# Optimization experiments

Measured on AMD Instinct MI355X. Metric: run time of the kernel, lower is better.

Reference implementation:

```python
import jax, jax.numpy as jnp
import numpy as np

N_STEPS = 20  # ceil((t1-t0)/dt0) with dt0=0.05 on [0,1]


def setup_inputs() -> dict:
    key = jax.random.key(0)
    ks = jax.random.split(key, 12)
    B, D, H, VF, LS, LAB = 512, 5, 128, 256, 63, 10
    Lm1 = LS - 1  # 62, effective logsig dim after dropping channel 0
    ts = jnp.linspace(0.0, 1.0, 33, dtype=jnp.float32)
    intervals = jnp.linspace(0.0, 1.0, 33, dtype=jnp.float32)
    logsig = jax.random.normal(ks[0], (32, LS), dtype=jnp.float32)
    x0 = jax.random.normal(ks[1], (B, D), dtype=jnp.float32)
    def lin(k, fan_in, shape):
        return jax.random.uniform(k, shape, jnp.float32, -1.0, 1.0) / np.sqrt(fan_in)
    return {
        "ts": ts, "logsig": logsig, "x0": x0, "intervals": intervals,
        "W_vf1": lin(ks[2], H, (VF, H)),  "b_vf1": lin(ks[3], H, (VF,)),
        "W_vf2": lin(ks[4], VF, (VF, VF)), "b_vf2": lin(ks[5], VF, (VF,)),
        "W_m": lin(ks[6], VF, (H * Lm1, VF)), "b_m": lin(ks[7], VF, (H * Lm1,)),
        "W_in": lin(ks[8], D, (H, D)),   "b_in": lin(ks[9], D, (H,)),
        "W_out": lin(ks[10], H, (LAB, H)), "b_out": lin(ks[11], H, (LAB,)),
    }


def reference(ts, logsig, x0, intervals, W_vf1, b_vf1, W_vf2, b_vf2,
              W_m, b_m, W_in, b_in, W_out, b_out):
    B = x0.shape[0]
    H = W_in.shape[0]
    L = logsig.shape[1] - 1  # channel 0 dropped

    def vector_field(t, y):
        # locate interval containing t (torch.searchsorted default = left)
        idx = jnp.clip(jnp.searchsorted(intervals[1:], t) + 1, 1, intervals.shape[0] - 1)
        seg = logsig[idx - 1, 1:]                     # (L,)
        h = jax.nn.relu(y @ W_vf1.T + b_vf1)          # (B, VF)
        h = jnp.tanh(h @ W_vf2.T + b_vf2)             # (B, VF) final_activation=tanh
        m = (h @ W_m.T + b_m).reshape(B, H, L)        # (B, H, L)
        dydt = jnp.einsum('bhl,l->bh', m, seg)
        return dydt / (intervals[idx] - intervals[idx - 1])

    y0 = x0 @ W_in.T + b_in                           # linear1
    t0, t1 = ts[0], ts[-1]
    dt = (t1 - t0) / N_STEPS

    def heun_step(y, i):
        t = t0 + i * dt
        k1 = vector_field(t, y)
        k2 = vector_field(t + dt, y + dt * k1)
        return y + 0.5 * dt * (k1 + k2), None

    yT, _ = jax.lax.scan(heun_step, y0, jnp.arange(N_STEPS, dtype=jnp.float32))
    return jax.nn.softmax(yT @ W_out.T + b_out, axis=-1)
```

## Files before the change

### kernel.cpp

```cpp
#include <hip/hip_runtime.h>

#define YW 136

typedef _Float16 f16x8 __attribute__((ext_vector_type(8)));
typedef _Float16 f16x4 __attribute__((ext_vector_type(4)));
typedef __attribute__((ext_vector_type(4))) float f32x4;

__device__ __forceinline__ float fast_tanh(float x) {
    float e = __expf(2.0f * x);
    return 1.0f - 2.0f / (e + 1.0f);
}
__device__ __forceinline__ void bar_lds() {
    asm volatile("s_waitcnt lgkmcnt(0)\n\ts_barrier" ::: "memory");
}

__device__ __forceinline__ int fidx(int m, int c) {
    return ((c >> 5) << 9) | (((c >> 3) & 3) << 7) | (m << 3) | (c & 7);
}

__global__ __launch_bounds__(512) void pk_all(
    const float* __restrict__ Wvf1, const float* __restrict__ Wvf2,
    const float* __restrict__ Wm,   const float* __restrict__ bm,
    const float* __restrict__ logsig,
    _Float16* __restrict__ W1F, _Float16* __restrict__ W2F,
    _Float16* __restrict__ A3F, float* __restrict__ c_all)
{
    __shared__ float ls[8][62];
    const int b = blockIdx.x, t = threadIdx.x;
    if (b < 16) {
        int u0 = (b * 512 + t) * 4;
        int j0 = u0 & 7, l = (u0 >> 3) & 63;
        int kc = (u0 >> 9) & 3, nt = u0 >> 11;
        int n = nt * 16 + (l & 15), k0 = kc * 32 + (l >> 4) * 8 + j0;
        f32x4 w = *(const f32x4*)(Wvf1 + n * 128 + k0);
        f16x4 hv, lv;
#pragma unroll
        for (int c = 0; c < 4; c++) {
            _Float16 hi = (_Float16)w[c];
            hv[c] = hi;
            lv[c] = (_Float16)(w[c] - (float)hi);
        }
        *(f16x4*)(W1F + u0) = hv;
        *(f16x4*)(W1F + 32768 + u0) = lv;
    } else if (b < 48) {
        int u0 = ((b - 16) * 512 + t) * 4;
        int j0 = u0 & 7, l = (u0 >> 3) & 63;
        int kc = (u0 >> 9) & 7, nt = u0 >> 12;
        int n = nt * 16 + (l & 15), k0 = kc * 32 + (l >> 4) * 8 + j0;
        f32x4 w = *(const f32x4*)(Wvf2 + n * 256 + k0);
        f16x4 hv, lv;
#pragma unroll
        for (int c = 0; c < 4; c++) {
            _Float16 hi = (_Float16)w[c];
            hv[c] = hi;
            lv[c] = (_Float16)(w[c] - (float)hi);
        }
        *(f16x4*)(W2F + u0) = hv;
        *(f16x4*)(W2F + 65536 + u0) = lv;
    } else if (b < 112) {
        int tid = (b - 48) * 512 + t;
        int chunk = tid >> 13;
        int qi = tid & 8191;
        int u0 = qi * 4;
        int r0 = chunk * 8;
        for (int e2 = t; e2 < 8 * 62; e2 += 512)
            ls[e2 / 62][e2 % 62] = logsig[(r0 + e2 / 62) * 63 + 1 + (e2 % 62)];
        __syncthreads();
        int j0 = u0 & 7, l = (u0 >> 3) & 63, kc = (u0 >> 9) & 7, nt = (u0 >> 12) & 7;
        int h = nt * 16 + (l & 15);
        int v0 = kc * 32 + (l >> 4) * 8 + j0;
        f32x4 acc[8];
#pragma unroll
        for (int r = 0; r < 8; r++) acc[r] = (f32x4){0.f, 0.f, 0.f, 0.f};
        const float* wp = Wm + h * 62 * 256 + v0;
#pragma unroll 2
        for (int ll = 0; ll < 62; ll++) {
            f32x4 w4 = *(const f32x4*)(wp + ll * 256);
#pragma unroll
            for (int r = 0; r < 8; r++) {
                float lsv = ls[r][ll];
#pragma unroll
                for (int c = 0; c < 4; c++)
                    acc[r][c] += w4[c] * lsv;
            }
        }
#pragma unroll
        for (int r = 0; r < 8; r++) {
            f16x4 hv, lv;
#pragma unroll
            for (int c = 0; c < 4; c++) {
                _Float16 hi = (_Float16)acc[r][c];
                hv[c] = hi;
                lv[c] = (_Float16)(acc[r][c] - (float)hi);
            }
            *(f16x4*)(A3F + (r0 + r) * 65536 + u0) = hv;
            *(f16x4*)(A3F + (r0 + r) * 65536 + 32768 + u0) = lv;
        }
    } else {
        int u = (b - 112) * 512 + t;
        int r = u >> 7, h = u & 127;
        float acc = 0.f;
#pragma unroll
        for (int ll = 0; ll < 62; ll++) acc += bm[h * 62 + ll] * logsig[r * 63 + 1 + ll];
        c_all[u] = acc;
    }
}

__global__ __launch_bounds__(512, 2) void rde_main(
    const float* __restrict__ ts, const float* __restrict__ x0,
    const float* __restrict__ intervals,
    const float* __restrict__ b1g, const float* __restrict__ b2g,
    const float* __restrict__ Win, const float* __restrict__ bin,
    const float* __restrict__ Wout, const float* __restrict__ bout,
    const _Float16* __restrict__ W1F, const _Float16* __restrict__ W2F,
    const _Float16* __restrict__ A3F, const float* __restrict__ c_all,
    float* __restrict__ out)
{
    __shared__ __align__(16) _Float16 W1s[32768];
    __shared__ __align__(16) _Float16 H1h[4096];
    __shared__ __align__(16) _Float16 H2h[4096];
    __shared__ __align__(16) _Float16 Yh[2048];
    __shared__ __align__(16) _Float16 Yl[2048];
    __shared__ float ivl[33];
    __shared__ int   r_arr[40];
    __shared__ float s_arr[40];

    const int t    = threadIdx.x;
    const int lane = t & 63;
    const int wv   = t >> 6;
    const int m16  = lane & 15;
    const int q    = lane >> 4;
    const int row0 = blockIdx.x * 16;

    if (t < 33) ivl[t] = intervals[t];
    for (int e2 = t; e2 < 4096; e2 += 512)
        ((uint4*)W1s)[e2] = ((const uint4*)W1F)[e2];
    __syncthreads();

    const float ts0 = ts[0];
    const float dt  = __fdiv_rn(ts[32] - ts0, 20.0f);

    if (t < 40) {
        int i = t >> 1;
        float tv = ts0 + (float)i * dt;
        if (t & 1) tv += dt;
        int p = 0;
        for (int j2 = 0; j2 < 32; j2++) p += (ivl[1 + j2] < tv) ? 1 : 0;
        int idx = p + 1;
        idx = idx < 1 ? 1 : idx;
        idx = idx > 32 ? 32 : idx;
        r_arr[t] = idx - 1;
        s_arr[t] = __fdiv_rn(1.0f, ivl[idx] - ivl[idx - 1]);
    }

    f32x4 b1f[2], b2f[2];
#pragma unroll
    for (int tt = 0; tt < 2; tt++) {
        b1f[tt] = *(const f32x4*)(b1g + (wv * 2 + tt) * 16 + q * 4);
        b2f[tt] = *(const f32x4*)(b2g + (wv * 2 + tt) * 16 + q * 4);
    }

    float Y[4], K1[4];
    {
        const float* xr = x0 + (row0 + m16) * 5;
        float xv[5];
#pragma unroll
        for (int d = 0; d < 5; d++) xv[d] = xr[d];
        int c0 = wv * 16 + q * 4;
        f16x4 hv, lv;
#pragma unroll
        for (int r = 0; r < 4; r++) {
            float acc = bin[c0 + r];
#pragma unroll
            for (int d = 0; d < 5; d++) acc += xv[d] * Win[(c0 + r) * 5 + d];
            Y[r] = acc;
            K1[r] = 0.f;
            _Float16 hi = (_Float16)acc;
            hv[r] = hi;
            lv[r] = (_Float16)(acc - (float)hi);
        }
        *(f16x4*)(Yh + fidx(m16, c0)) = hv;
        *(f16x4*)(Yl + fidx(m16, c0)) = lv;
    }

    f16x8 w1lo[2][4];
#pragma unroll
    for (int tt = 0; tt < 2; tt++)
#pragma unroll
        for (int kc = 0; kc < 4; kc++)
            w1lo[tt][kc] = *(const f16x8*)(W1F + 32768 + ((wv * 8 + tt * 4 + kc) * 64 + lane) * 8);
    __syncthreads();

#pragma unroll 1
    for (int e = 0; e < 40; e++) {
        const int half = e & 1;
        const int ri   = r_arr[e];
        const float s  = s_arr[e];
        const _Float16* ABase = A3F + ri * 65536;

        f16x8 w2a[2][4][2];
#pragma unroll
        for (int tt = 0; tt < 2; tt++)
#pragma unroll
            for (int kc = 0; kc < 4; kc++) {
                const _Float16* bp = W2F + ((wv * 16 + tt * 8 + kc) * 64 + lane) * 8;
                w2a[tt][kc][0] = *(const f16x8*)bp;
                w2a[tt][kc][1] = *(const f16x8*)(bp + 65536);
            }
        f32x4 aA[2], aB[2], aC[2];
#pragma unroll
        for (int tt = 0; tt < 2; tt++) {
            aA[tt] = b1f[tt];
            aB[tt] = (f32x4){0.f, 0.f, 0.f, 0.f};
            aC[tt] = (f32x4){0.f, 0.f, 0.f, 0.f};
        }
#pragma unroll
        for (int kc = 0; kc < 4; kc++) {
            f16x8 ah = *(const f16x8*)(Yh + kc * 512 + lane * 8);
            f16x8 al = *(const f16x8*)(Yl + kc * 512 + lane * 8);
#pragma unroll
            for (int tt = 0; tt < 2; tt++) {
                f16x8 bh = *(const f16x8*)(W1s + ((wv * 8 + tt * 4 + kc) * 64 + lane) * 8);
                aA[tt] = __builtin_amdgcn_mfma_f32_16x16x32_f16(bh, ah, aA[tt], 0, 0, 0);
                aB[tt] = __builtin_amdgcn_mfma_f32_16x16x32_f16(w1lo[tt][kc], ah, aB[tt], 0, 0, 0);
                aC[tt] = __builtin_amdgcn_mfma_f32_16x16x32_f16(bh, al, aC[tt], 0, 0, 0);
            }
        }
#pragma unroll
        for (int tt = 0; tt < 2; tt++) {
            int n0 = (wv * 2 + tt) * 16 + q * 4;
            f16x4 hv;
#pragma unroll
            for (int r = 0; r < 4; r++)
                hv[r] = (_Float16)fmaxf(aA[tt][r] + aB[tt][r] + aC[tt][r], 0.f);
            *(f16x4*)(H1h + fidx(m16, n0)) = hv;
        }
        bar_lds();

        f16x8 w2b[2][4][2];
#pragma unroll
        for (int tt = 0; tt < 2; tt++)
#pragma unroll
            for (int kc = 0; kc < 4; kc++) {
                const _Float16* bp = W2F + ((wv * 16 + tt * 8 + 4 + kc) * 64 + lane) * 8;
                w2b[tt][kc][0] = *(const f16x8*)bp;
                w2b[tt][kc][1] = *(const f16x8*)(bp + 65536);
            }
#pragma unroll
        for (int tt = 0; tt < 2; tt++) {
            aA[tt] = b2f[tt];
            aB[tt] = (f32x4){0.f, 0.f, 0.f, 0.f};
        }
#pragma unroll
        for (int kc = 0; kc < 4; kc++) {
            f16x8 ah = *(const f16x8*)(H1h + kc * 512 + lane * 8);
#pragma unroll
            for (int tt = 0; tt < 2; tt++) {
                aA[tt] = __builtin_amdgcn_mfma_f32_16x16x32_f16(w2a[tt][kc][0], ah, aA[tt], 0, 0, 0);
                aB[tt] = __builtin_amdgcn_mfma_f32_16x16x32_f16(w2a[tt][kc][1], ah, aB[tt], 0, 0, 0);
            }
        }
        f16x8 a3a[4][2];
#pragma unroll
        for (int kc = 0; kc < 4; kc++) {
            const _Float16* bp = ABase + ((wv * 8 + kc) * 64 + lane) * 8;
            a3a[kc][0] = *(const f16x8*)bp;
            a3a[kc][1] = *(const f16x8*)(bp + 32768);
        }
        f32x4 cf = *(const f32x4*)(c_all + ri * 128 + wv * 16 + q * 4);
#pragma unroll
        for (int kc = 0; kc < 4; kc++) {
            f16x8 ah = *(const f16x8*)(H1h + (4 + kc) * 512 + lane * 8);
#pragma unroll
            for (int tt = 0; tt < 2; tt++) {
                aA[tt] = __builtin_amdgcn_mfma_f32_16x16x32_f16(w2b[tt][kc][0], ah, aA[tt], 0, 0, 0);
                aB[tt] = __builtin_amdgcn_mfma_f32_16x16x32_f16(w2b[tt][kc][1], ah, aB[tt], 0, 0, 0);
            }
        }
        f16x8 a3b[4][2];
#pragma unroll
        for (int kc = 0; kc < 4; kc++) {
            const _Float16* bp = ABase + ((wv * 8 + 4 + kc) * 64 + lane) * 8;
            a3b[kc][0] = *(const f16x8*)bp;
            a3b[kc][1] = *(const f16x8*)(bp + 32768);
        }
#pragma unroll
        for (int tt = 0; tt < 2; tt++) {
            int n0 = (wv * 2 + tt) * 16 + q * 4;
            f16x4 hv;
#pragma unroll
            for (int r = 0; r < 4; r++)
                hv[r] = (_Float16)fast_tanh(aA[tt][r] + aB[tt][r]);
            *(f16x4*)(H2h + fidx(m16, n0)) = hv;
        }
        bar_lds();

        f32x4 kA = cf;
        f32x4 kB = (f32x4){0.f, 0.f, 0.f, 0.f};
#pragma unroll
        for (int kc = 0; kc < 4; kc++) {
            f16x8 ah = *(const f16x8*)(H2h + kc * 512 + lane * 8);
            kA = __builtin_amdgcn_mfma_f32_16x16x32_f16(a3a[kc][0], ah, kA, 0, 0, 0);
            kB = __builtin_amdgcn_mfma_f32_16x16x32_f16(a3a[kc][1], ah, kB, 0, 0, 0);
        }
#pragma unroll
        for (int kc = 0; kc < 4; kc++) {
            f16x8 ah = *(const f16x8*)(H2h + (4 + kc) * 512 + lane * 8);
            kA = __builtin_amdgcn_mfma_f32_16x16x32_f16(a3b[kc][0], ah, kA, 0, 0, 0);
            kB = __builtin_amdgcn_mfma_f32_16x16x32_f16(a3b[kc][1], ah, kB, 0, 0, 0);
        }
#pragma unroll
        for (int tt = 0; tt < 2; tt++)
#pragma unroll
            for (int kc = 0; kc < 4; kc++)
                w1lo[tt][kc] = *(const f16x8*)(W1F + 32768 + ((wv * 8 + tt * 4 + kc) * 64 + lane) * 8);
        {
            int c0 = wv * 16 + q * 4;
            f16x4 hv, lv;
#pragma unroll
            for (int r = 0; r < 4; r++) {
                float kv = (kA[r] + kB[r]) * s;
                float yn;
                if (half == 0) {
                    K1[r] = kv;
                    yn = Y[r] + dt * kv;
                } else {
                    yn = Y[r] + 0.5f * dt * (K1[r] + kv);
                    Y[r] = yn;
                }
                _Float16 hi = (_Float16)yn;
                hv[r] = hi;
                lv[r] = (_Float16)(yn - (float)hi);
            }
            *(f16x4*)(Yh + fidx(m16, c0)) = hv;
            *(f16x4*)(Yl + fidx(m16, c0)) = lv;
        }
        bar_lds();
    }

    float* Ys  = (float*)&W1s[0];
    float* lgp = (float*)&W1s[0] + 16 * YW;
#pragma unroll
    for (int r = 0; r < 4; r++)
        Ys[m16 * YW + wv * 16 + q * 4 + r] = Y[r];
    __syncthreads();
    if (t < 160) {
        int m = t / 10, c = t % 10;
        float acc = bout[c];
        for (int k = 0; k < 128; k++) acc += Ys[m * YW + k] * Wout[c * 128 + k];
        lgp[m * 10 + c] = acc;
    }
    __syncthreads();
    if (t < 16) {
        float mx = -1e30f;
#pragma unroll
        for (int c = 0; c < 10; c++) mx = fmaxf(mx, lgp[t * 10 + c]);
        float ex[10], sum = 0.f;
#pragma unroll
        for (int c = 0; c < 10; c++) { ex[c] = expf(lgp[t * 10 + c] - mx); sum += ex[c]; }
        float inv = __fdiv_rn(1.0f, sum);
#pragma unroll
        for (int c = 0; c < 10; c++) out[(row0 + t) * 10 + c] = ex[c] * inv;
    }
}

extern "C" void kernel_launch(void* const* d_in, const int* in_sizes, int n_in,
                              void* d_out, int out_size, void* d_ws, size_t ws_size,
                              hipStream_t stream) {
    const float* ts     = (const float*)d_in[0];
    const float* logsig = (const float*)d_in[1];
    const float* x0     = (const float*)d_in[2];
    const float* ivls   = (const float*)d_in[3];
    const float* Wvf1   = (const float*)d_in[4];
    const float* bvf1   = (const float*)d_in[5];
    const float* Wvf2   = (const float*)d_in[6];
    const float* bvf2   = (const float*)d_in[7];
    const float* Wm     = (const float*)d_in[8];
    const float* bm     = (const float*)d_in[9];
    const float* Win    = (const float*)d_in[10];
    const float* bin    = (const float*)d_in[11];
    const float* Wout   = (const float*)d_in[12];
    const float* bout   = (const float*)d_in[13];

    _Float16* W1F = (_Float16*)d_ws;
    _Float16* W2F = W1F + 65536;
    _Float16* A3F = W2F + 131072;
    float* c_all = (float*)(A3F + 32 * 65536);
    float* out = (float*)d_out;

    pk_all<<<dim3(120), dim3(512), 0, stream>>>(Wvf1, Wvf2, Wm, bm, logsig,
                                                W1F, W2F, A3F, c_all);
    rde_main<<<dim3(32), dim3(512), 0, stream>>>(
        ts, x0, ivls, bvf1, bvf2, Win, bin, Wout, bout,
        W1F, W2F, A3F, c_all, out);
}
```

Measured before the change: 243.9 us.

## Fuse weight-packing prologue into main RDE kernel via cooperative grid sync

```diff
diff --git a/kernel.cpp b/kernel.cpp
--- a/kernel.cpp
+++ b/kernel.cpp
@@ -1,4 +1,7 @@
 #include <hip/hip_runtime.h>
+#include <hip/hip_cooperative_groups.h>
+
+namespace cg = cooperative_groups;
 
 #define YW 136
 
@@ -18,102 +21,17 @@
     return ((c >> 5) << 9) | (((c >> 3) & 3) << 7) | (m << 3) | (c & 7);
 }
 
-__global__ __launch_bounds__(512) void pk_all(
-    const float* __restrict__ Wvf1, const float* __restrict__ Wvf2,
-    const float* __restrict__ Wm,   const float* __restrict__ bm,
-    const float* __restrict__ logsig,
-    _Float16* __restrict__ W1F, _Float16* __restrict__ W2F,
-    _Float16* __restrict__ A3F, float* __restrict__ c_all)
-{
-    __shared__ float ls[8][62];
-    const int b = blockIdx.x, t = threadIdx.x;
-    if (b < 16) {
-        int u0 = (b * 512 + t) * 4;
-        int j0 = u0 & 7, l = (u0 >> 3) & 63;
-        int kc = (u0 >> 9) & 3, nt = u0 >> 11;
-        int n = nt * 16 + (l & 15), k0 = kc * 32 + (l >> 4) * 8 + j0;
-        f32x4 w = *(const f32x4*)(Wvf1 + n * 128 + k0);
-        f16x4 hv, lv;
-#pragma unroll
-        for (int c = 0; c < 4; c++) {
-            _Float16 hi = (_Float16)w[c];
-            hv[c] = hi;
-            lv[c] = (_Float16)(w[c] - (float)hi);
-        }
-        *(f16x4*)(W1F + u0) = hv;
-        *(f16x4*)(W1F + 32768 + u0) = lv;
-    } else if (b < 48) {
-        int u0 = ((b - 16) * 512 + t) * 4;
-        int j0 = u0 & 7, l = (u0 >> 3) & 63;
-        int kc = (u0 >> 9) & 7, nt = u0 >> 12;
-        int n = nt * 16 + (l & 15), k0 = kc * 32 + (l >> 4) * 8 + j0;
-        f32x4 w = *(const f32x4*)(Wvf2 + n * 256 + k0);
-        f16x4 hv, lv;
-#pragma unroll
-        for (int c = 0; c < 4; c++) {
-            _Float16 hi = (_Float16)w[c];
-            hv[c] = hi;
-            lv[c] = (_Float16)(w[c] - (float)hi);
-        }
-        *(f16x4*)(W2F + u0) = hv;
-        *(f16x4*)(W2F + 65536 + u0) = lv;
-    } else if (b < 112) {
-        int tid = (b - 48) * 512 + t;
-        int chunk = tid >> 13;
-        int qi = tid & 8191;
-        int u0 = qi * 4;
-        int r0 = chunk * 8;
-        for (int e2 = t; e2 < 8 * 62; e2 += 512)
-            ls[e2 / 62][e2 % 62] = logsig[(r0 + e2 / 62) * 63 + 1 + (e2 % 62)];
-        __syncthreads();
-        int j0 = u0 & 7, l = (u0 >> 3) & 63, kc = (u0 >> 9) & 7, nt = (u0 >> 12) & 7;
-        int h = nt * 16 + (l & 15);
-        int v0 = kc * 32 + (l >> 4) * 8 + j0;
-        f32x4 acc[8];
-#pragma unroll
-        for (int r = 0; r < 8; r++) acc[r] = (f32x4){0.f, 0.f, 0.f, 0.f};
-        const float* wp = Wm + h * 62 * 256 + v0;
-#pragma unroll 2
-        for (int ll = 0; ll < 62; ll++) {
-            f32x4 w4 = *(const f32x4*)(wp + ll * 256);
-#pragma unroll
-            for (int r = 0; r < 8; r++) {
-                float lsv = ls[r][ll];
-#pragma unroll
-                for (int c = 0; c < 4; c++)
-                    acc[r][c] += w4[c] * lsv;
-            }
-        }
-#pragma unroll
-        for (int r = 0; r < 8; r++) {
-            f16x4 hv, lv;
-#pragma unroll
-            for (int c = 0; c < 4; c++) {
-                _Float16 hi = (_Float16)acc[r][c];
-                hv[c] = hi;
-                lv[c] = (_Float16)(acc[r][c] - (float)hi);
-            }
-            *(f16x4*)(A3F + (r0 + r) * 65536 + u0) = hv;
-            *(f16x4*)(A3F + (r0 + r) * 65536 + 32768 + u0) = lv;
-        }
-    } else {
-        int u = (b - 112) * 512 + t;
-        int r = u >> 7, h = u & 127;
-        float acc = 0.f;
-#pragma unroll
-        for (int ll = 0; ll < 62; ll++) acc += bm[h * 62 + ll] * logsig[r * 63 + 1 + ll];
-        c_all[u] = acc;
-    }
-}
-
-__global__ __launch_bounds__(512, 2) void rde_main(
+__global__ __launch_bounds__(512, 2) void rde_fused(
     const float* __restrict__ ts, const float* __restrict__ x0,
     const float* __restrict__ intervals,
     const float* __restrict__ b1g, const float* __restrict__ b2g,
     const float* __restrict__ Win, const float* __restrict__ bin,
     const float* __restrict__ Wout, const float* __restrict__ bout,
-    const _Float16* __restrict__ W1F, const _Float16* __restrict__ W2F,
-    const _Float16* __restrict__ A3F, const float* __restrict__ c_all,
+    const float* __restrict__ Wvf1, const float* __restrict__ Wvf2,
+    const float* __restrict__ Wm,   const float* __restrict__ bm,
+    const float* __restrict__ logsig,
+    _Float16* __restrict__ W1LO, _Float16* __restrict__ W2F,
+    _Float16* __restrict__ A3F, float* __restrict__ c_all,
     float* __restrict__ out)
 {
     __shared__ __align__(16) _Float16 W1s[32768];
@@ -130,11 +48,91 @@
     const int wv   = t >> 6;
     const int m16  = lane & 15;
     const int q    = lane >> 4;
-    const int row0 = blockIdx.x * 16;
+    const int b    = blockIdx.x;
+    const int row0 = b * 16;
+
+    float* ls32 = (float*)H1h;
+    for (int e2 = t; e2 < 32 * 62; e2 += 512)
+        ls32[e2] = logsig[(e2 / 62) * 63 + 1 + (e2 % 62)];
+
+    {
+        int u0 = (b * 512 + t) * 4;
+        int j0 = u0 & 7, l = (u0 >> 3) & 63;
+        int kc = (u0 >> 9) & 7, nt = u0 >> 12;
+        int n = nt * 16 + (l & 15), k0 = kc * 32 + (l >> 4) * 8 + j0;
+        f32x4 w = *(const f32x4*)(Wvf2 + n * 256 + k0);
+        f16x4 hv, lv;
+#pragma unroll
+        for (int c = 0; c < 4; c++) {
+            _Float16 hi = (_Float16)w[c];
+            hv[c] = hi;
+            lv[c] = (_Float16)(w[c] - (float)hi);
+        }
+        *(f16x4*)(W2F + u0) = hv;
+        *(f16x4*)(W2F + 65536 + u0) = lv;
+    }
+    for (int u = t; u < 32768; u += 512) {
+        int j = u & 7, l = (u >> 3) & 63, kc = (u >> 9) & 3, nt = u >> 11;
+        int n = nt * 16 + (l & 15), k = kc * 32 + (l >> 4) * 8 + j;
+        W1s[u] = (_Float16)Wvf1[n * 128 + k];
+    }
+    for (int u = b * 1024 + t; u < (b + 1) * 1024; u += 512) {
+        int j = u & 7, l = (u >> 3) & 63, kc = (u >> 9) & 3, nt = u >> 11;
+        int n = nt * 16 + (l & 15), k = kc * 32 + (l >> 4) * 8 + j;
+        float w = Wvf1[n * 128 + k];
+        _Float16 hi = (_Float16)w;
+        W1LO[u] = (_Float16)(w - (float)hi);
+    }
+    if (t < 128) {
+        float acc = 0.f;
+#pragma unroll
+        for (int ll = 0; ll < 62; ll++)
+            acc += bm[t * 62 + ll] * logsig[b * 63 + 1 + ll];
+        c_all[b * 128 + t] = acc;
+    }
+    __syncthreads();
+
+    {
+        int qd = b * 256 + (t & 255);
+        int rh = t >> 8;
+        int u0 = qd * 4;
+        int j0 = u0 & 7, l = (u0 >> 3) & 63, kc = (u0 >> 9) & 7, nt = (u0 >> 12) & 7;
+        int h = nt * 16 + (l & 15);
+        int v0 = kc * 32 + (l >> 4) * 8 + j0;
+        f32x4 acc[16];
+#pragma unroll
+        for (int r = 0; r < 16; r++) acc[r] = (f32x4){0.f, 0.f, 0.f, 0.f};
+        const float* wp  = Wm + h * 62 * 256 + v0;
+        const float* lsp = ls32 + (rh * 16) * 62;
+#pragma unroll 2
+        for (int ll = 0; ll < 62; ll++) {
+            f32x4 w4 = *(const f32x4*)(wp + ll * 256);
+#pragma unroll
+            for (int r = 0; r < 16; r++) {
+                float lsv = lsp[r * 62 + ll];
+#pragma unroll
+                for (int c = 0; c < 4; c++)
+                    acc[r][c] += w4[c] * lsv;
+            }
+        }
+#pragma unroll
+        for (int r = 0; r < 16; r++) {
+            f16x4 hv, lv;
+#pragma unroll
+            for (int c = 0; c < 4; c++) {
+                _Float16 hi = (_Float16)acc[r][c];
+                hv[c] = hi;
+                lv[c] = (_Float16)(acc[r][c] - (float)hi);
+            }
+            *(f16x4*)(A3F + (rh * 16 + r) * 65536 + u0) = hv;
+            *(f16x4*)(A3F + (rh * 16 + r) * 65536 + 32768 + u0) = lv;
+        }
+    }
+
+    __threadfence();
+    cg::this_grid().sync();
 
     if (t < 33) ivl[t] = intervals[t];
-    for (int e2 = t; e2 < 4096; e2 += 512)
-        ((uint4*)W1s)[e2] = ((const uint4*)W1F)[e2];
     __syncthreads();
 
     const float ts0 = ts[0];
@@ -188,7 +186,7 @@
     for (int tt = 0; tt < 2; tt++)
 #pragma unroll
         for (int kc = 0; kc < 4; kc++)
-            w1lo[tt][kc] = *(const f16x8*)(W1F + 32768 + ((wv * 8 + tt * 4 + kc) * 64 + lane) * 8);
+            w1lo[tt][kc] = *(const f16x8*)(W1LO + ((wv * 8 + tt * 4 + kc) * 64 + lane) * 8);
     __syncthreads();
 
 #pragma unroll 1
@@ -313,7 +311,7 @@
         for (int tt = 0; tt < 2; tt++)
 #pragma unroll
             for (int kc = 0; kc < 4; kc++)
-                w1lo[tt][kc] = *(const f16x8*)(W1F + 32768 + ((wv * 8 + tt * 4 + kc) * 64 + lane) * 8);
+                w1lo[tt][kc] = *(const f16x8*)(W1LO + ((wv * 8 + tt * 4 + kc) * 64 + lane) * 8);
         {
             int c0 = wv * 16 + q * 4;
             f16x4 hv, lv;
@@ -382,15 +380,20 @@
     const float* Wout   = (const float*)d_in[12];
     const float* bout   = (const float*)d_in[13];
 
-    _Float16* W1F = (_Float16*)d_ws;
-    _Float16* W2F = W1F + 65536;
-    _Float16* A3F = W2F + 131072;
-    float* c_all = (float*)(A3F + 32 * 65536);
-    float* out = (float*)d_out;
-
-    pk_all<<<dim3(120), dim3(512), 0, stream>>>(Wvf1, Wvf2, Wm, bm, logsig,
-                                                W1F, W2F, A3F, c_all);
-    rde_main<<<dim3(32), dim3(512), 0, stream>>>(
-        ts, x0, ivls, bvf1, bvf2, Win, bin, Wout, bout,
-        W1F, W2F, A3F, c_all, out);
-}
+    _Float16* W1LO  = (_Float16*)d_ws;
+    _Float16* W2F   = W1LO + 32768;
+    _Float16* A3F   = W2F + 131072;
+    float*    c_all = (float*)(A3F + 32 * 65536);
+    float*    out   = (float*)d_out;
+
+    void* args[] = {
+        (void*)&ts, (void*)&x0, (void*)&ivls,
+        (void*)&bvf1, (void*)&bvf2, (void*)&Win, (void*)&bin,
+        (void*)&Wout, (void*)&bout,
+        (void*)&Wvf1, (void*)&Wvf2, (void*)&Wm, (void*)&bm, (void*)&logsig,
+        (void*)&W1LO, (void*)&W2F, (void*)&A3F, (void*)&c_all,
+        (void*)&out
+    };
+    hipLaunchCooperativeKernel((const void*)rde_fused, dim3(32), dim3(512),
+                               args, 0, stream);
+}
```

Measured after the change: 296.0 us. +21.4%, slower.
